# Kernel tuning notes

Hardware: AMD Instinct MI355X
Metric: run time of the kernel (lower is better)

Reference implementation:

```python
import jax, jax.numpy as jnp
import numpy as np

B, S, I, H, O = 64, 2048, 256, 512, 10

def setup_inputs() -> dict:
    key = jax.random.key(0)
    ks = jax.random.split(key, 16)
    s_in = 1.0 / np.sqrt(I)
    s_h = 1.0 / np.sqrt(H)
    return {
        "x": jax.random.normal(ks[0], (B, S, I), dtype=jnp.float32),
        "Wz": jax.random.normal(ks[1], (H, I), dtype=jnp.float32) * s_in,
        "bz": jax.random.normal(ks[2], (H,), dtype=jnp.float32) * s_in,
        "Uz": jax.random.normal(ks[3], (H, H), dtype=jnp.float32) * s_h,
        "cz": jax.random.normal(ks[4], (H,), dtype=jnp.float32) * s_h,
        "Wr": jax.random.normal(ks[5], (H, I), dtype=jnp.float32) * s_in,
        "br": jax.random.normal(ks[6], (H,), dtype=jnp.float32) * s_in,
        "Ur": jax.random.normal(ks[7], (H, H), dtype=jnp.float32) * s_h,
        "cr": jax.random.normal(ks[8], (H,), dtype=jnp.float32) * s_h,
        "Wh": jax.random.normal(ks[9], (H, I), dtype=jnp.float32) * s_in,
        "bh": jax.random.normal(ks[10], (H,), dtype=jnp.float32) * s_in,
        "Uh": jax.random.normal(ks[11], (H, H), dtype=jnp.float32) * s_h,
        "ch": jax.random.normal(ks[12], (H,), dtype=jnp.float32) * s_h,
        "Wf": jax.random.normal(ks[13], (O, H), dtype=jnp.float32) * s_h,
        "bf": jax.random.normal(ks[14], (O,), dtype=jnp.float32) * s_h,
    }


def reference(x, Wz, bz, Uz, cz, Wr, br, Ur, cr, Wh, bh, Uh, ch, Wf, bf):
    b, s, _ = x.shape
    h_dim = Uz.shape[0]
    # Precompute input-gate projections for all timesteps in 3 big GEMMs: [B,S,H]
    xz = jnp.einsum('bsi,hi->bsh', x, Wz) + bz
    xr = jnp.einsum('bsi,hi->bsh', x, Wr) + br
    xh = jnp.einsum('bsi,hi->bsh', x, Wh) + bh
    # scan over time (transpose to time-major [S,B,H])
    xs = (jnp.swapaxes(xz, 0, 1), jnp.swapaxes(xr, 0, 1), jnp.swapaxes(xh, 0, 1))

    def step(h, ins):
        xz_t, xr_t, xh_t = ins
        z = jax.nn.sigmoid(xz_t + h @ Uz.T + cz)
        r = jax.nn.sigmoid(xr_t + h @ Ur.T + cr)
        h_tilde = jnp.tanh(xh_t + (r * h) @ Uh.T + ch)
        h_new = (1.0 - z) * h + z * h_tilde
        return h_new, None

    h0 = jnp.zeros((b, h_dim), dtype=x.dtype)
    h_T, _ = jax.lax.scan(step, h0, xs)
    return h_T @ Wf.T + bf
```

## Files before the change

### kernel.cpp

```cpp
#include <hip/hip_runtime.h>
#include <stdint.h>


#define S_LEN  2048
#define BATCH  64
#define IDIM   256
#define HDIM   512
#define ODIM   10
#define GATES3 1536

typedef __attribute__((ext_vector_type(8))) short bf16x8;
typedef __attribute__((ext_vector_type(4))) float f32x4;

__device__ __forceinline__ unsigned short f2bf(float x) {
    unsigned int u = __float_as_uint(x);
    u += 0x7fffu + ((u >> 16) & 1u);
    return (unsigned short)(u >> 16);
}
__device__ __forceinline__ float bf2f(unsigned short h) {
    return __uint_as_float(((unsigned int)h) << 16);
}

__device__ __forceinline__ unsigned long long g_load64(const void* p) {
    return __hip_atomic_load((const unsigned long long*)p, __ATOMIC_RELAXED, __HIP_MEMORY_SCOPE_AGENT);
}
__device__ __forceinline__ void g_store32(void* p, unsigned int v) {
    __hip_atomic_store((unsigned int*)p, v, __ATOMIC_RELAXED, __HIP_MEMORY_SCOPE_AGENT);
}

__global__ __launch_bounds__(256)
void proj_mfma(const float* __restrict__ x,
               const float* __restrict__ Wz, const float* __restrict__ Wr, const float* __restrict__ Wh,
               const float* __restrict__ bz, const float* __restrict__ cz,
               const float* __restrict__ br, const float* __restrict__ cr,
               const float* __restrict__ bh, const float* __restrict__ ch,
               unsigned short* __restrict__ xp2)
{
    __shared__ unsigned short As[8 * 128 * 8];
    __shared__ unsigned short Bs[8 * 128 * 8];
    const int tid  = threadIdx.x;
    const int wave = tid >> 6;
    const int lane = tid & 63;
    const int quad = lane >> 4;
    const int l16  = lane & 15;
    const int nt_ = blockIdx.x;
    const int mt_ = blockIdx.y;

    const int srow  = tid >> 1;
    const int shalf = tid & 1;
    const int mg = mt_ * 128 + srow;
    const float* axrow = x + ((size_t)(mg & 63) * S_LEN + (mg >> 6)) * IDIM + shalf * 32;
    const int ng = nt_ * 128 + srow;
    const int gt = ng >> 9, hl = ng & 511;
    const float* bxrow = (gt == 0 ? Wz : gt == 1 ? Wr : Wh) + (size_t)hl * IDIM + shalf * 32;

    f32x4 acc[2][8];
#pragma unroll
    for (int mi = 0; mi < 2; ++mi)
#pragma unroll
        for (int nj = 0; nj < 8; ++nj) {
            f32x4 z = {0.f, 0.f, 0.f, 0.f};
            acc[mi][nj] = z;
        }

    for (int kp = 0; kp < IDIM; kp += 64) {
#pragma unroll
        for (int c = 0; c < 4; ++c) {
            unsigned short ta[8], tb[8];
#pragma unroll
            for (int e = 0; e < 8; ++e) {
                ta[e] = f2bf(axrow[kp + c * 8 + e]);
                tb[e] = f2bf(bxrow[kp + c * 8 + e]);
            }
            const int kcq = shalf * 4 + c;
            *(bf16x8*)(As + (kcq * 128 + srow) * 8) = *(bf16x8*)ta;
            *(bf16x8*)(Bs + (kcq * 128 + srow) * 8) = *(bf16x8*)tb;
        }
        __syncthreads();
#pragma unroll
        for (int kc = 0; kc < 2; ++kc) {
            bf16x8 af[2], bfr[8];
#pragma unroll
            for (int mi = 0; mi < 2; ++mi)
                af[mi] = *(const bf16x8*)(As + ((kc * 4 + quad) * 128 + wave * 32 + mi * 16 + l16) * 8);
#pragma unroll
            for (int nj = 0; nj < 8; ++nj)
                bfr[nj] = *(const bf16x8*)(Bs + ((kc * 4 + quad) * 128 + nj * 16 + l16) * 8);
#pragma unroll
            for (int mi = 0; mi < 2; ++mi)
#pragma unroll
                for (int nj = 0; nj < 8; ++nj)
                    acc[mi][nj] = __builtin_amdgcn_mfma_f32_16x16x32_bf16(af[mi], bfr[nj], acc[mi][nj], 0, 0, 0);
        }
        __syncthreads();
    }

    const int s_ = mt_ * 2 + (wave >> 1);
#pragma unroll
    for (int nj = 0; nj < 8; ++nj) {
        const int n  = nt_ * 128 + nj * 16 + l16;
        const int g2 = n >> 9, h2 = n & 511;
        const float bias = (g2 == 0 ? bz[h2] + cz[h2]
                          : g2 == 1 ? br[h2] + cr[h2]
                                    : bh[h2] + ch[h2]);
#pragma unroll
        for (int mi = 0; mi < 2; ++mi) {
            const int gg = (wave & 1) * 2 + mi;
            unsigned short pk[4];
#pragma unroll
            for (int r = 0; r < 4; ++r) pk[r] = f2bf(acc[mi][nj][r] + bias);
            *(unsigned long long*)(xp2 + (((size_t)gg * S_LEN + s_) * GATES3 + n) * 16 + quad * 4) =
                *(unsigned long long*)pk;
        }
    }
}

__device__ __forceinline__ void stage_frag(const unsigned short* __restrict__ gsrc,
                                           unsigned short* __restrict__ lds, int tid)
{
    unsigned long long v[8];
#pragma unroll
    for (int i = 0; i < 8; ++i) v[i] = g_load64(gsrc + (tid + i * 256) * 4);
    unsigned long long* q = (unsigned long long*)lds;
#pragma unroll
    for (int i = 0; i < 8; ++i) q[tid + i * 256] = v[i];
}

__device__ __forceinline__ void group_barrier(unsigned int* __restrict__ flags, int g, int j,
                                              unsigned int epoch, int tid, int lane)
{
    __syncthreads();
    if (tid == 0)
        __hip_atomic_store(&flags[(g * 16 + j) * 16], epoch,
                           __ATOMIC_RELAXED, __HIP_MEMORY_SCOPE_AGENT);
    if (lane < 16) {
        const unsigned int* f = &flags[(g * 16 + lane) * 16];
        while (__hip_atomic_load(f, __ATOMIC_RELAXED, __HIP_MEMORY_SCOPE_AGENT) < epoch)
            __builtin_amdgcn_s_sleep(2);
    }
}

__global__ __launch_bounds__(256)
void gru_recur(const float* __restrict__ Uz, const float* __restrict__ Ur,
               const float* __restrict__ Uh,
               const unsigned short* __restrict__ xp2,
               unsigned short* __restrict__ hg,
               unsigned short* __restrict__ rhg,
               float* __restrict__ hgf,
               unsigned int* __restrict__ flags,
               const float* __restrict__ Wf, const float* __restrict__ bfv,
               float* __restrict__ out)
{
    __shared__ unsigned short ldsA[8192];
    __shared__ unsigned short ldsB[8192];
    __shared__ float hlds[16][33];
    const int tid  = threadIdx.x;
    const int wave = tid >> 6;
    const int lane = tid & 63;
    const int quad = lane >> 4;
    const int l16  = lane & 15;
    const int g  = blockIdx.x & 3;
    const int j  = blockIdx.x >> 2;
    const int b0 = g * 16;
    const int i0 = j * 32;
    const int nt = wave & 1;
    const bool isZ = (wave < 2);

    for (int i = tid; i < 16 * 33; i += 256) (&hlds[0][0])[i] = 0.f;

    const int wrow = i0 + nt * 16 + l16;
    const int kofs = quad * 8;
    bf16x8 wp1[16], wp2[16];
    const float* U1 = isZ ? Uz : Ur;
#pragma unroll
    for (int kb = 0; kb < 16; ++kb) {
        const float* s1 = U1 + (size_t)wrow * HDIM + kb * 32 + kofs;
        const float* s2 = Uh + (size_t)wrow * HDIM + kb * 32 + kofs;
        bf16x8 w1, w2;
#pragma unroll
        for (int e = 0; e < 8; ++e) {
            w1[e] = (short)f2bf(s1[e]);
            w2[e] = (short)f2bf(s2[e]);
        }
        wp1[kb] = w1; wp2[kb] = w2;
    }

    const int iloc = nt * 16 + l16;
    const int icol = i0 + iloc;
    const int pidx = (icol >> 5) * 512 + ((icol >> 3) & 3) * 128 + (icol & 7);
    unsigned short* hgG  = hg  + g * 8192;
    unsigned short* rhgG = rhg + g * 8192;
    const unsigned short* xpg = xp2 + (size_t)g * S_LEN * GATES3 * 16;
    const int gofs1 = isZ ? 0 : HDIM;

    float zfrag[4];
    float hm[4] = {0.f, 0.f, 0.f, 0.f};

    unsigned long long xg_cur = *(const unsigned long long*)
        (xpg + ((size_t)0 * GATES3 + gofs1 + icol) * 16 + quad * 4);
    unsigned long long xh_cur = *(const unsigned long long*)
        (xpg + ((size_t)0 * GATES3 + 2 * HDIM + icol) * 16 + quad * 4);

    __syncthreads();

    for (int t = 0; t < S_LEN; ++t) {
        stage_frag(hgG, ldsA, tid);
        __syncthreads();

        f32x4 c1 = {0.f, 0.f, 0.f, 0.f};
#pragma unroll
        for (int kb = 0; kb < 16; ++kb) {
            const bf16x8 a = *(const bf16x8*)(ldsA + kb * 512 + quad * 128 + l16 * 8);
            c1 = __builtin_amdgcn_mfma_f32_16x16x32_bf16(a, wp1[kb], c1, 0, 0, 0);
        }
        union { unsigned long long q; unsigned short s[4]; } xq;
        xq.q = xg_cur;
        if (isZ) {
#pragma unroll
            for (int r = 0; r < 4; ++r) {
                const float pre = c1[r] + bf2f(xq.s[r]);
                zfrag[r] = 1.f / (1.f + __expf(-pre));
            }
        } else {
#pragma unroll
            for (int r = 0; r < 4; ++r) {
                const float pre = c1[r] + bf2f(xq.s[r]);
                const float v = 1.f / (1.f + __expf(-pre));
                const float rh = v * hlds[quad * 4 + r][iloc];
                unsigned int my = f2bf(rh);
                unsigned int other = (unsigned int)__shfl_xor((int)my, 1, 64);
                if ((lane & 1) == 0)
                    g_store32(rhgG + pidx + (quad * 4 + r) * 8, my | (other << 16));
            }
        }
        group_barrier(flags, g, j, 2u * (unsigned)t + 1u, tid, lane);

        stage_frag(rhgG, ldsB, tid);
        __syncthreads();

        if (isZ) {
            f32x4 c2 = {0.f, 0.f, 0.f, 0.f};
#pragma unroll
            for (int kb = 0; kb < 16; ++kb) {
                const bf16x8 a = *(const bf16x8*)(ldsB + kb * 512 + quad * 128 + l16 * 8);
                c2 = __builtin_amdgcn_mfma_f32_16x16x32_bf16(a, wp2[kb], c2, 0, 0, 0);
            }
            union { unsigned long long q; unsigned short s[4]; } xh;
            xh.q = xh_cur;
            float hn[4];
#pragma unroll
            for (int r = 0; r < 4; ++r) {
                const float pre = c2[r] + bf2f(xh.s[r]);
                const float ht = tanhf(pre);
                hn[r] = hm[r] + zfrag[r] * (ht - hm[r]);
                hm[r] = hn[r];
            }
#pragma unroll
            for (int r = 0; r < 4; ++r) {
                unsigned int my = f2bf(hn[r]);
                unsigned int other = (unsigned int)__shfl_xor((int)my, 1, 64);
                if ((lane & 1) == 0)
                    g_store32(hgG + pidx + (quad * 4 + r) * 8, my | (other << 16));
            }
#pragma unroll
            for (int r = 0; r < 4; ++r) {
                hlds[quad * 4 + r][iloc] = hn[r];
                if (t == S_LEN - 1)
                    g_store32(hgf + (size_t)(b0 + quad * 4 + r) * HDIM + icol,
                              __float_as_uint(hn[r]));
            }
        }
        const int tn = (t + 1 < S_LEN) ? t + 1 : t;
        xg_cur = *(const unsigned long long*)
            (xpg + ((size_t)tn * GATES3 + gofs1 + icol) * 16 + quad * 4);
        xh_cur = *(const unsigned long long*)
            (xpg + ((size_t)tn * GATES3 + 2 * HDIM + icol) * 16 + quad * 4);

        group_barrier(flags, g, j, 2u * (unsigned)t + 2u, tid, lane);
    }

    if (j == 0 && tid < 16 * ODIM) {
        const int b = b0 + tid / ODIM;
        const int o = tid % ODIM;
        float acc = bfv[o];
        for (int k = 0; k < HDIM; k += 2) {
            union { unsigned long long q; float f[2]; } w;
            w.q = g_load64(hgf + (size_t)b * HDIM + k);
            acc += w.f[0] * Wf[o * HDIM + k] + w.f[1] * Wf[o * HDIM + k + 1];
        }
        out[b * ODIM + o] = acc;
    }
}

extern "C" void kernel_launch(void* const* d_in, const int* in_sizes, int n_in,
                              void* d_out, int out_size, void* d_ws, size_t ws_size,
                              hipStream_t stream)
{
    const float* x  = (const float*)d_in[0];
    const float* Wz = (const float*)d_in[1];
    const float* bz = (const float*)d_in[2];
    const float* Uz = (const float*)d_in[3];
    const float* cz = (const float*)d_in[4];
    const float* Wr = (const float*)d_in[5];
    const float* br = (const float*)d_in[6];
    const float* Ur = (const float*)d_in[7];
    const float* cr = (const float*)d_in[8];
    const float* Wh = (const float*)d_in[9];
    const float* bh = (const float*)d_in[10];
    const float* Uh = (const float*)d_in[11];
    const float* ch = (const float*)d_in[12];
    const float* Wf = (const float*)d_in[13];
    const float* bf = (const float*)d_in[14];
    float* out = (float*)d_out;

    char* ws = (char*)d_ws;
    const size_t XPB = (size_t)S_LEN * BATCH * GATES3 * sizeof(unsigned short);
    unsigned short* xp2 = (unsigned short*)ws;
    unsigned short* hg  = (unsigned short*)(ws + XPB);
    unsigned short* rhg = (unsigned short*)(ws + XPB + 65536);
    float*          hgf = (float*)(ws + XPB + 131072);
    unsigned int*   flg = (unsigned int*)(ws + XPB + 262144);

    hipMemsetAsync(ws + XPB, 0, 262144 + 4096, stream);

    proj_mfma<<<dim3(12, 1024), 256, 0, stream>>>(
        x, Wz, Wr, Wh, bz, cz, br, cr, bh, ch, xp2);

    gru_recur<<<dim3(64), dim3(256), 0, stream>>>(
        Uz, Ur, Uh, xp2, hg, rhg, hgf, flg, Wf, bf, out);
}
```

Baseline: 9.537 ms.

## Replace flag barriers with epoch-tagged double-buffered hidden-state exchange

Removes the two per-timestep flag barriers between the 16 blocks of each batch group. Each 32-bit bf16 pair of h and r*h is now stored together with the timestep epoch in a 64-bit word, in double-buffered global arrays. Consumers poll-load the whole fragment and use __syncthreads_and to check that every word carries the expected epoch before continuing. This cuts a flag store/spin round trip per phase, but doubles the bytes moved per step and retries the full fragment load whenever any word is stale.

```diff
diff --git a/kernel.cpp b/kernel.cpp
--- a/kernel.cpp
+++ b/kernel.cpp
@@ -24,8 +24,14 @@
 __device__ __forceinline__ unsigned long long g_load64(const void* p) {
     return __hip_atomic_load((const unsigned long long*)p, __ATOMIC_RELAXED, __HIP_MEMORY_SCOPE_AGENT);
 }
+__device__ __forceinline__ void g_store64(void* p, unsigned long long v) {
+    __hip_atomic_store((unsigned long long*)p, v, __ATOMIC_RELAXED, __HIP_MEMORY_SCOPE_AGENT);
+}
 __device__ __forceinline__ void g_store32(void* p, unsigned int v) {
     __hip_atomic_store((unsigned int*)p, v, __ATOMIC_RELAXED, __HIP_MEMORY_SCOPE_AGENT);
+}
+__device__ __forceinline__ unsigned int g_load32(const void* p) {
+    return __hip_atomic_load((const unsigned int*)p, __ATOMIC_RELAXED, __HIP_MEMORY_SCOPE_AGENT);
 }
 
 __global__ __launch_bounds__(256)
@@ -115,28 +121,19 @@
     }
 }
 
-__device__ __forceinline__ void stage_frag(const unsigned short* __restrict__ gsrc,
-                                           unsigned short* __restrict__ lds, int tid)
+__device__ __forceinline__ void stage_epoch(const unsigned long long* __restrict__ src,
+                                            unsigned int* __restrict__ lds32, int tid,
+                                            unsigned int expect)
 {
-    unsigned long long v[8];
-#pragma unroll
-    for (int i = 0; i < 8; ++i) v[i] = g_load64(gsrc + (tid + i * 256) * 4);
-    unsigned long long* q = (unsigned long long*)lds;
-#pragma unroll
-    for (int i = 0; i < 8; ++i) q[tid + i * 256] = v[i];
-}
-
-__device__ __forceinline__ void group_barrier(unsigned int* __restrict__ flags, int g, int j,
-                                              unsigned int epoch, int tid, int lane)
-{
-    __syncthreads();
-    if (tid == 0)
-        __hip_atomic_store(&flags[(g * 16 + j) * 16], epoch,
-                           __ATOMIC_RELAXED, __HIP_MEMORY_SCOPE_AGENT);
-    if (lane < 16) {
-        const unsigned int* f = &flags[(g * 16 + lane) * 16];
-        while (__hip_atomic_load(f, __ATOMIC_RELAXED, __HIP_MEMORY_SCOPE_AGENT) < epoch)
-            __builtin_amdgcn_s_sleep(2);
+    for (;;) {
+        int ok = 1;
+#pragma unroll
+        for (int i = 0; i < 16; ++i) {
+            const unsigned long long v = g_load64(src + tid + i * 256);
+            lds32[tid + i * 256] = (unsigned int)v;
+            ok &= ((unsigned int)(v >> 32) == expect) ? 1 : 0;
+        }
+        if (__syncthreads_and(ok)) break;
     }
 }
 
@@ -144,15 +141,15 @@
 void gru_recur(const float* __restrict__ Uz, const float* __restrict__ Ur,
                const float* __restrict__ Uh,
                const unsigned short* __restrict__ xp2,
-               unsigned short* __restrict__ hg,
-               unsigned short* __restrict__ rhg,
+               unsigned long long* __restrict__ hb,
+               unsigned long long* __restrict__ rb,
                float* __restrict__ hgf,
                unsigned int* __restrict__ flags,
                const float* __restrict__ Wf, const float* __restrict__ bfv,
                float* __restrict__ out)
 {
-    __shared__ unsigned short ldsA[8192];
-    __shared__ unsigned short ldsB[8192];
+    __shared__ unsigned int ldsA32[4096];
+    __shared__ unsigned int ldsB32[4096];
     __shared__ float hlds[16][33];
     const int tid  = threadIdx.x;
     const int wave = tid >> 6;
@@ -187,9 +184,9 @@
 
     const int iloc = nt * 16 + l16;
     const int icol = i0 + iloc;
-    const int pidx = (icol >> 5) * 512 + ((icol >> 3) & 3) * 128 + (icol & 7);
-    unsigned short* hgG  = hg  + g * 8192;
-    unsigned short* rhgG = rhg + g * 8192;
+    const int wbase = (icol >> 5) * 256 + ((icol >> 3) & 3) * 64 + ((icol & 7) >> 1);
+    unsigned long long* hbG = hb + (size_t)g * 4096;
+    unsigned long long* rbG = rb + (size_t)g * 4096;
     const unsigned short* xpg = xp2 + (size_t)g * S_LEN * GATES3 * 16;
     const int gofs1 = isZ ? 0 : HDIM;
 
@@ -204,13 +201,13 @@
     __syncthreads();
 
     for (int t = 0; t < S_LEN; ++t) {
-        stage_frag(hgG, ldsA, tid);
-        __syncthreads();
+        const unsigned int epNew = (unsigned)t + 1u;
+        stage_epoch(hbG + (size_t)(((t + 1) & 1) * 4) * 4096, ldsA32, tid, (unsigned)t);
 
         f32x4 c1 = {0.f, 0.f, 0.f, 0.f};
 #pragma unroll
         for (int kb = 0; kb < 16; ++kb) {
-            const bf16x8 a = *(const bf16x8*)(ldsA + kb * 512 + quad * 128 + l16 * 8);
+            const bf16x8 a = *(const bf16x8*)((const unsigned short*)ldsA32 + kb * 512 + quad * 128 + l16 * 8);
             c1 = __builtin_amdgcn_mfma_f32_16x16x32_bf16(a, wp1[kb], c1, 0, 0, 0);
         }
         union { unsigned long long q; unsigned short s[4]; } xq;
@@ -222,6 +219,7 @@
                 zfrag[r] = 1.f / (1.f + __expf(-pre));
             }
         } else {
+            unsigned long long* rbP = rbG + (size_t)((t & 1) * 4) * 4096;
 #pragma unroll
             for (int r = 0; r < 4; ++r) {
                 const float pre = c1[r] + bf2f(xq.s[r]);
@@ -230,19 +228,19 @@
                 unsigned int my = f2bf(rh);
                 unsigned int other = (unsigned int)__shfl_xor((int)my, 1, 64);
                 if ((lane & 1) == 0)
-                    g_store32(rhgG + pidx + (quad * 4 + r) * 8, my | (other << 16));
-            }
-        }
-        group_barrier(flags, g, j, 2u * (unsigned)t + 1u, tid, lane);
-
-        stage_frag(rhgG, ldsB, tid);
-        __syncthreads();
+                    g_store64(rbP + wbase + (quad * 4 + r) * 4,
+                              (unsigned long long)(my | (other << 16)) |
+                              ((unsigned long long)epNew << 32));
+            }
+        }
+
+        stage_epoch(rbG + (size_t)((t & 1) * 4) * 4096, ldsB32, tid, epNew);
 
         if (isZ) {
             f32x4 c2 = {0.f, 0.f, 0.f, 0.f};
 #pragma unroll
             for (int kb = 0; kb < 16; ++kb) {
-                const bf16x8 a = *(const bf16x8*)(ldsB + kb * 512 + quad * 128 + l16 * 8);
+                const bf16x8 a = *(const bf16x8*)((const unsigned short*)ldsB32 + kb * 512 + quad * 128 + l16 * 8);
                 c2 = __builtin_amdgcn_mfma_f32_16x16x32_bf16(a, wp2[kb], c2, 0, 0, 0);
             }
             union { unsigned long long q; unsigned short s[4]; } xh;
@@ -255,12 +253,15 @@
                 hn[r] = hm[r] + zfrag[r] * (ht - hm[r]);
                 hm[r] = hn[r];
             }
+            unsigned long long* hbP = hbG + (size_t)((t & 1) * 4) * 4096;
 #pragma unroll
             for (int r = 0; r < 4; ++r) {
                 unsigned int my = f2bf(hn[r]);
                 unsigned int other = (unsigned int)__shfl_xor((int)my, 1, 64);
                 if ((lane & 1) == 0)
-                    g_store32(hgG + pidx + (quad * 4 + r) * 8, my | (other << 16));
+                    g_store64(hbP + wbase + (quad * 4 + r) * 4,
+                              (unsigned long long)(my | (other << 16)) |
+                              ((unsigned long long)epNew << 32));
             }
 #pragma unroll
             for (int r = 0; r < 4; ++r) {
@@ -275,20 +276,28 @@
             (xpg + ((size_t)tn * GATES3 + gofs1 + icol) * 16 + quad * 4);
         xh_cur = *(const unsigned long long*)
             (xpg + ((size_t)tn * GATES3 + 2 * HDIM + icol) * 16 + quad * 4);
-
-        group_barrier(flags, g, j, 2u * (unsigned)t + 2u, tid, lane);
-    }
-
-    if (j == 0 && tid < 16 * ODIM) {
-        const int b = b0 + tid / ODIM;
-        const int o = tid % ODIM;
-        float acc = bfv[o];
-        for (int k = 0; k < HDIM; k += 2) {
-            union { unsigned long long q; float f[2]; } w;
-            w.q = g_load64(hgf + (size_t)b * HDIM + k);
-            acc += w.f[0] * Wf[o * HDIM + k] + w.f[1] * Wf[o * HDIM + k + 1];
-        }
-        out[b * ODIM + o] = acc;
+    }
+
+    __syncthreads();
+    if (tid == 0) g_store32(&flags[(g * 16 + j) * 16], 1u);
+    if (j == 0) {
+        if (lane < 16) {
+            const unsigned int* f = &flags[(g * 16 + lane) * 16];
+            while (g_load32(f) < 1u)
+                __builtin_amdgcn_s_sleep(2);
+        }
+        __syncthreads();
+        if (tid < 16 * ODIM) {
+            const int b = b0 + tid / ODIM;
+            const int o = tid % ODIM;
+            float acc = bfv[o];
+            for (int k = 0; k < HDIM; k += 2) {
+                union { unsigned long long q; float f[2]; } w;
+                w.q = g_load64(hgf + (size_t)b * HDIM + k);
+                acc += w.f[0] * Wf[o * HDIM + k] + w.f[1] * Wf[o * HDIM + k + 1];
+            }
+            out[b * ODIM + o] = acc;
+        }
     }
 }
 
@@ -315,17 +324,17 @@
 
     char* ws = (char*)d_ws;
     const size_t XPB = (size_t)S_LEN * BATCH * GATES3 * sizeof(unsigned short);
-    unsigned short* xp2 = (unsigned short*)ws;
-    unsigned short* hg  = (unsigned short*)(ws + XPB);
-    unsigned short* rhg = (unsigned short*)(ws + XPB + 65536);
-    float*          hgf = (float*)(ws + XPB + 131072);
-    unsigned int*   flg = (unsigned int*)(ws + XPB + 262144);
-
-    hipMemsetAsync(ws + XPB, 0, 262144 + 4096, stream);
+    unsigned short*     xp2 = (unsigned short*)ws;
+    unsigned long long* hb  = (unsigned long long*)(ws + XPB);
+    unsigned long long* rb  = (unsigned long long*)(ws + XPB + 262144);
+    float*              hgf = (float*)(ws + XPB + 524288);
+    unsigned int*       flg = (unsigned int*)(ws + XPB + 655360);
+
+    hipMemsetAsync(ws + XPB, 0, 524288 + 131072 + 4096, stream);
 
     proj_mfma<<<dim3(12, 1024), 256, 0, stream>>>(
         x, Wz, Wr, Wh, bz, cz, br, cr, bh, ch, xp2);
 
     gru_recur<<<dim3(64), dim3(256), 0, stream>>>(
-        Uz, Ur, Uh, xp2, hg, rhg, hgf, flg, Wf, bf, out);
-}
+        Uz, Ur, Uh, xp2, hb, rb, hgf, flg, Wf, bf, out);
+}
```

New measurement: 28.84 ms. 3.02x slower.
